# Performance work log

Measured on AMD Instinct MI355X. Metric: run time of the kernel, lower is better.

Reference implementation:

```python
import jax, jax.numpy as jnp
import numpy as np

N = 50000; E = 800000; H = 4; C = 64; FEAT = 128; EDIM = 16; G = 256
NEG_SLOPE = 0.2; BN_EPS = 1e-5


def _gat_layer(x, src, dst, W, a_src, a_dst, bias, gamma, beta, alpha_edge=None):
    # GATConv (concat=True, PyG math), then BatchNorm1d (batch stats) + ReLU.
    h = (x @ W).reshape(N, H, C)                       # [N,H,C]
    alpha = (h * a_src).sum(-1)[src] + (h * a_dst).sum(-1)[dst]   # [Etot,H]
    if alpha_edge is not None:
        alpha = alpha + alpha_edge
    alpha = jax.nn.leaky_relu(alpha, NEG_SLOPE)
    amax = jax.ops.segment_max(alpha, dst, num_segments=N)        # edge softmax over dst
    ea = jnp.exp(alpha - amax[dst])
    denom = jax.ops.segment_sum(ea, dst, num_segments=N)
    coef = ea / (denom[dst] + 1e-16)
    out = jax.ops.segment_sum(coef[:, :, None] * h[src], dst, num_segments=N)
    out = out.reshape(N, H * C) + bias
    mu = out.mean(0)
    var = out.var(0)
    out = (out - mu) / jnp.sqrt(var + BN_EPS) * gamma + beta
    return jax.nn.relu(out)


def setup_inputs() -> dict:
    key = jax.random.key(0)
    ks = jax.random.split(key, 32)
    s = 0.05
    inp = {
        "x": jax.random.normal(ks[0], (N, FEAT), jnp.float32),
        "edge_index": jax.random.randint(ks[1], (2, E), 0, N),
        "edge_attr": jax.random.normal(ks[2], (E, EDIM), jnp.float32),
        "batch": jnp.sort(jax.random.randint(ks[3], (N,), 0, G)),
    }
    in_dims = [FEAT, H * C, H * C]
    for i in range(3):
        k = 4 + 7 * i
        inp[f"W{i}"] = jax.random.normal(ks[k], (in_dims[i], H * C), jnp.float32) * s
        inp[f"att_src{i}"] = jax.random.normal(ks[k + 1], (H, C), jnp.float32) * s
        inp[f"att_dst{i}"] = jax.random.normal(ks[k + 2], (H, C), jnp.float32) * s
        inp[f"bias{i}"] = jnp.zeros((H * C,), jnp.float32)
        inp[f"gamma{i}"] = jnp.ones((H * C,), jnp.float32)
        inp[f"beta{i}"] = jnp.zeros((H * C,), jnp.float32)
    inp["We0"] = jax.random.normal(ks[28], (EDIM, H * C), jnp.float32) * s
    inp["att_e0"] = jax.random.normal(ks[29], (H, C), jnp.float32) * s
    return inp


def reference(x, edge_index, edge_attr, batch,
              W0, att_src0, att_dst0, bias0, gamma0, beta0,
              W1, att_src1, att_dst1, bias1, gamma1, beta1,
              W2, att_src2, att_dst2, bias2, gamma2, beta2,
              We0, att_e0):
    # PyG GATConv adds self-loops; edge_attr for self-loops filled with mean.
    loops = jnp.arange(N)
    src = jnp.concatenate([edge_index[0], loops])
    dst = jnp.concatenate([edge_index[1], loops])
    ea_sl = jnp.concatenate([edge_attr, jnp.broadcast_to(edge_attr.mean(0), (N, EDIM))], 0)
    e = (ea_sl @ We0).reshape(E + N, H, C)
    alpha_e = (e * att_e0).sum(-1)                     # [Etot,H]
    x = _gat_layer(x, src, dst, W0, att_src0, att_dst0, bias0, gamma0, beta0, alpha_e)
    x = _gat_layer(x, src, dst, W1, att_src1, att_dst1, bias1, gamma1, beta1)
    x = _gat_layer(x, src, dst, W2, att_src2, att_dst2, bias2, gamma2, beta2)
    # global_mean_pool
    counts = jax.ops.segment_sum(jnp.ones((N,), x.dtype), batch, num_segments=G)
    sums = jax.ops.segment_sum(x, batch, num_segments=G)
    return sums / jnp.clip(counts, 1.0)[:, None]
```

## Files before the change

kernel.cpp:

```cpp
#include <hip/hip_runtime.h>
#include <math.h>

#define NN 50000
#define NE 800000
#define ET 850000
#define HCC 256
#define GG 256
#define CAP 64
#define NB 16

constexpr size_t NHC    = (size_t)NN * HCC;
constexpr size_t O_H    = 0;
constexpr size_t O_AGG  = O_H + NHC / 2;
constexpr size_t O_REC  = O_AGG + NHC / 2;
constexpr size_t O_BT0  = O_REC + (size_t)NN * CAP * 4;
constexpr size_t O_BT1  = O_BT0 + 16384;
constexpr size_t O_BT2  = O_BT1 + 32768;
constexpr size_t O_AS   = O_BT2 + 32768;
constexpr size_t O_AD   = O_AS + (size_t)NN * 4;
constexpr size_t O_M    = O_AD + (size_t)NN * 4;
constexpr size_t O_ZERO = O_M + 64;
constexpr size_t O_DEG  = O_ZERO;
constexpr size_t O_SLS  = O_DEG + NN;
constexpr size_t O_PART = O_SLS + 4;
constexpr size_t O_END  = O_PART + 3 * NB * 512;

typedef __attribute__((ext_vector_type(8))) short bf16x8;
typedef __attribute__((ext_vector_type(4))) float f32x4;

__device__ inline unsigned short f2bf(float f) {
    unsigned int u = __float_as_uint(f);
    unsigned int r = (u + 0x7fffu + ((u >> 16) & 1u)) >> 16;
    return (unsigned short)r;
}
__device__ inline float b2f(unsigned short u) {
    return __uint_as_float(((unsigned int)u) << 16);
}
__device__ inline float bflo(unsigned int u) { return __uint_as_float(u << 16); }
__device__ inline float bfhi(unsigned int u) { return __uint_as_float(u & 0xffff0000u); }

__global__ void prep_kernel(const float* __restrict__ W0, const float* __restrict__ W1,
                            const float* __restrict__ W2,
                            const float* __restrict__ We0, const float* __restrict__ att_e0,
                            unsigned short* __restrict__ Bt0,
                            unsigned short* __restrict__ Bt1,
                            unsigned short* __restrict__ Bt2,
                            float* __restrict__ M) {
    int b = blockIdx.x;
    if (b == 640) {
        int t = threadIdx.x;
        if (t < 64) {
            int k = t >> 2, hh = t & 3;
            float s = 0.f;
            for (int c = 0; c < 64; ++c)
                s += We0[k * 256 + hh * 64 + c] * att_e0[hh * 64 + c];
            M[k * 4 + hh] = s;
        }
        return;
    }
    const float* W; unsigned short* Bt; int K, base;
    if (b < 128)      { W = W0; Bt = Bt0; K = 128; base = 0; }
    else if (b < 384) { W = W1; Bt = Bt1; K = 256; base = 128; }
    else              { W = W2; Bt = Bt2; K = 256; base = 384; }
    int idx = (b - base) * 256 + threadIdx.x;
    int n = idx & 255, k = idx >> 8;
    Bt[(size_t)n * K + k] = f2bf(W[(size_t)k * 256 + n]);
}

__global__ void csr_kernel(const int* __restrict__ srcA, const int* __restrict__ dstA,
                           const float* __restrict__ ea, const float* __restrict__ M,
                           int* __restrict__ deg, uint4* __restrict__ rec,
                           float* __restrict__ slsum) {
    int t0 = blockIdx.x * 1024 + threadIdx.x;
    float a0 = 0.f, a1 = 0.f, a2 = 0.f, a3 = 0.f;
    #pragma unroll
    for (int q = 0; q < 4; ++q) {
        int e = t0 + q * 256;
        if (e < ET) {
            bool real = (e < NE);
            int d = real ? dstA[e] : (e - NE);
            int s = real ? srcA[e] : (e - NE);
            int p = atomicAdd(&deg[d], 1);
            if (p > CAP - 1) p = CAP - 1;
            int slot = d * CAP + p;
            uint4 r;
            r.z = (unsigned)s;
            if (real) {
                r.w = 0u;
                const float4* pp = (const float4*)(ea + (size_t)e * 16);
                float4 va = pp[0], vb = pp[1], vc = pp[2], vd = pp[3];
                float v[16] = {va.x, va.y, va.z, va.w, vb.x, vb.y, vb.z, vb.w,
                               vc.x, vc.y, vc.z, vc.w, vd.x, vd.y, vd.z, vd.w};
                float o0 = 0.f, o1 = 0.f, o2 = 0.f, o3 = 0.f;
                #pragma unroll
                for (int k = 0; k < 16; ++k) {
                    float4 m4 = *(const float4*)(M + k * 4);
                    o0 = fmaf(v[k], m4.x, o0);
                    o1 = fmaf(v[k], m4.y, o1);
                    o2 = fmaf(v[k], m4.z, o2);
                    o3 = fmaf(v[k], m4.w, o3);
                }
                r.x = ((unsigned)f2bf(o1) << 16) | (unsigned)f2bf(o0);
                r.y = ((unsigned)f2bf(o3) << 16) | (unsigned)f2bf(o2);
                a0 += o0; a1 += o1; a2 += o2; a3 += o3;
            } else {
                r.x = 0u; r.y = 0u; r.w = 1u;
            }
            rec[slot] = r;
        }
    }
    #pragma unroll
    for (int off = 32; off; off >>= 1) {
        a0 += __shfl_xor(a0, off);
        a1 += __shfl_xor(a1, off);
        a2 += __shfl_xor(a2, off);
        a3 += __shfl_xor(a3, off);
    }
    __shared__ float part[4][4];
    int wave = threadIdx.x >> 6, lane = threadIdx.x & 63;
    if (lane == 0) {
        part[wave][0] = a0; part[wave][1] = a1;
        part[wave][2] = a2; part[wave][3] = a3;
    }
    __syncthreads();
    if (threadIdx.x < 4)
        atomicAdd(&slsum[threadIdx.x],
                  part[0][threadIdx.x] + part[1][threadIdx.x] +
                  part[2][threadIdx.x] + part[3][threadIdx.x]);
}

template <int K, bool NORM>
__global__ __launch_bounds__(256) void gemm_fused(const float* __restrict__ Af,
                                                  const unsigned short* __restrict__ Ab,
                                                  const unsigned short* __restrict__ Bt,
                                                  const float* __restrict__ part,
                                                  const float* __restrict__ gamma,
                                                  const float* __restrict__ beta,
                                                  const float* __restrict__ att_src,
                                                  const float* __restrict__ att_dst,
                                                  unsigned short* __restrict__ Hout,
                                                  float* __restrict__ asA,
                                                  float* __restrict__ adA, int M) {
    __shared__ unsigned short As[64][40];
    __shared__ unsigned short Bs[256][40];
    __shared__ float kvs[256], cvs[256];
    int tid = threadIdx.x;
    int wave = tid >> 6, lane = tid & 63;
    int quad = lane >> 4, l16 = lane & 15;
    int row0 = blockIdx.x * 64;
    f32x4 acc[4][4] = {};

    if (NORM) {
        int ch = tid;
        float s = 0.f, s2 = 0.f;
        #pragma unroll
        for (int b = 0; b < NB; ++b) {
            s  += part[b * 512 + ch];
            s2 += part[b * 512 + 256 + ch];
        }
        const float invN = 1.0f / (float)NN;
        float mr = s * invN;
        float var = s2 * invN - mr * mr;
        float k = gamma[ch] * rsqrtf(var + 1e-5f);
        kvs[ch] = k;
        cvs[ch] = beta[ch] - mr * k;
        __syncthreads();
    }

    for (int k0 = 0; k0 < K; k0 += 32) {
        {
            int row = tid >> 2, seg = tid & 3;
            ushort4 o0 = make_ushort4(0, 0, 0, 0), o1 = o0;
            if (row0 + row < M) {
                float u[8];
                if (NORM) {
                    uint4 raw = *(const uint4*)(Ab + (size_t)(row0 + row) * K + k0 + seg * 8);
                    u[0] = bflo(raw.x); u[1] = bfhi(raw.x);
                    u[2] = bflo(raw.y); u[3] = bfhi(raw.y);
                    u[4] = bflo(raw.z); u[5] = bfhi(raw.z);
                    u[6] = bflo(raw.w); u[7] = bfhi(raw.w);
                    int cb = k0 + seg * 8;
                    #pragma unroll
                    for (int q = 0; q < 8; ++q)
                        u[q] = fmaxf(fmaf(u[q], kvs[cb + q], cvs[cb + q]), 0.f);
                } else {
                    const float* ap = Af + (size_t)(row0 + row) * K + k0 + seg * 8;
                    float4 f1 = *(const float4*)ap;
                    float4 f2 = *(const float4*)(ap + 4);
                    u[0] = f1.x; u[1] = f1.y; u[2] = f1.z; u[3] = f1.w;
                    u[4] = f2.x; u[5] = f2.y; u[6] = f2.z; u[7] = f2.w;
                }
                o0 = make_ushort4(f2bf(u[0]), f2bf(u[1]), f2bf(u[2]), f2bf(u[3]));
                o1 = make_ushort4(f2bf(u[4]), f2bf(u[5]), f2bf(u[6]), f2bf(u[7]));
            }
            *(ushort4*)&As[row][seg * 8] = o0;
            *(ushort4*)&As[row][seg * 8 + 4] = o1;
        }
        {
            const uint4* src = (const uint4*)(Bt + (size_t)tid * K + k0);
            uint4 b0 = src[0], b1 = src[1], b2 = src[2], b3 = src[3];
            uint4* dst = (uint4*)&Bs[tid][0];
            dst[0] = b0; dst[1] = b1; dst[2] = b2; dst[3] = b3;
        }
        __syncthreads();
        bf16x8 a_frag[4], b_frag[4];
        #pragma unroll
        for (int mi = 0; mi < 4; ++mi)
            a_frag[mi] = *(const bf16x8*)&As[mi * 16 + l16][quad * 8];
        #pragma unroll
        for (int ni = 0; ni < 4; ++ni)
            b_frag[ni] = *(const bf16x8*)&Bs[wave * 64 + ni * 16 + l16][quad * 8];
        #pragma unroll
        for (int mi = 0; mi < 4; ++mi)
            #pragma unroll
            for (int ni = 0; ni < 4; ++ni)
                acc[mi][ni] = __builtin_amdgcn_mfma_f32_16x16x32_bf16(
                    a_frag[mi], b_frag[ni], acc[mi][ni], 0, 0, 0);
        __syncthreads();
    }

    #pragma unroll
    for (int mi = 0; mi < 4; ++mi) {
        #pragma unroll
        for (int reg = 0; reg < 4; ++reg) {
            int r = row0 + mi * 16 + quad * 4 + reg;
            if (r < M) {
                #pragma unroll
                for (int ni = 0; ni < 4; ++ni) {
                    int c = wave * 64 + ni * 16 + l16;
                    Hout[(size_t)r * HCC + c] = f2bf(acc[mi][ni][reg]);
                }
            }
        }
    }
    float asc[4], adc_[4];
    #pragma unroll
    for (int ni = 0; ni < 4; ++ni) {
        asc[ni] = att_src[wave * 64 + ni * 16 + l16];
        adc_[ni] = att_dst[wave * 64 + ni * 16 + l16];
    }
    #pragma unroll
    for (int mi = 0; mi < 4; ++mi) {
        #pragma unroll
        for (int reg = 0; reg < 4; ++reg) {
            float s1 = acc[mi][0][reg] * asc[0] + acc[mi][1][reg] * asc[1] +
                       acc[mi][2][reg] * asc[2] + acc[mi][3][reg] * asc[3];
            float d1 = acc[mi][0][reg] * adc_[0] + acc[mi][1][reg] * adc_[1] +
                       acc[mi][2][reg] * adc_[2] + acc[mi][3][reg] * adc_[3];
            #pragma unroll
            for (int off = 1; off < 16; off <<= 1) {
                s1 += __shfl_xor(s1, off);
                d1 += __shfl_xor(d1, off);
            }
            int r = row0 + mi * 16 + quad * 4 + reg;
            if (l16 == 0 && r < M) {
                asA[(size_t)r * 4 + wave] = s1;
                adA[(size_t)r * 4 + wave] = d1;
            }
        }
    }
}

template <bool HAS_AE>
__global__ __launch_bounds__(256) void agg_kernel(const unsigned short* __restrict__ Hm,
                                                  const float* __restrict__ asA,
                                                  const float* __restrict__ adA,
                                                  const uint4* __restrict__ rec,
                                                  const int* __restrict__ degA,
                                                  const float* __restrict__ slsum,
                                                  unsigned short* __restrict__ outA,
                                                  float* __restrict__ part) {
    __shared__ float wlds[4][260];
    __shared__ float slds[2][4][256];
    int wave = threadIdx.x >> 6, lane = threadIdx.x & 63;
    int n = blockIdx.x * 4 + wave;
    int head = lane >> 4;
    int st = n * CAP;
    int d = degA[n];
    if (d > CAP) d = CAP;
    float4 ad4 = *(const float4*)(adA + (size_t)n * 4);

    float4 w4 = make_float4(0.f, 0.f, 0.f, 0.f);
    int ms = 0;
    if (lane < d) {
        uint4 r = rec[st + lane];
        ms = (int)r.z;
        float4 av = *(const float4*)(asA + (size_t)ms * 4);
        float4 t = make_float4(av.x + ad4.x, av.y + ad4.y, av.z + ad4.z, av.w + ad4.w);
        if (HAS_AE) {
            if (r.w) {
                const float inv = 1.0f / (float)NE;
                t.x += slsum[0] * inv; t.y += slsum[1] * inv;
                t.z += slsum[2] * inv; t.w += slsum[3] * inv;
            } else {
                t.x += bflo(r.x); t.y += bfhi(r.x);
                t.z += bflo(r.y); t.w += bfhi(r.y);
            }
        }
        t.x = (t.x > 0.f) ? t.x : 0.2f * t.x;
        t.y = (t.y > 0.f) ? t.y : 0.2f * t.y;
        t.z = (t.z > 0.f) ? t.z : 0.2f * t.z;
        t.w = (t.w > 0.f) ? t.w : 0.2f * t.w;
        w4.x = __expf(t.x);
        w4.y = __expf(t.y);
        w4.z = __expf(t.z);
        w4.w = __expf(t.w);
    }
    float4 Dv = w4;
    wlds[wave][0 * 65 + lane] = w4.x;
    wlds[wave][1 * 65 + lane] = w4.y;
    wlds[wave][2 * 65 + lane] = w4.z;
    wlds[wave][3 * 65 + lane] = w4.w;

    float4 acc = make_float4(0.f, 0.f, 0.f, 0.f);
    const unsigned short* hb = Hm + lane * 4;
    int cnt8 = (d + 7) & ~7;
    const float* wrow = &wlds[wave][head * 65];
    for (int jj = 0; jj < cnt8; jj += 8) {
        int sj[8];
        #pragma unroll
        for (int q = 0; q < 8; ++q)
            sj[q] = __builtin_amdgcn_readlane(ms, jj + q);
        ushort4 hv[8];
        #pragma unroll
        for (int q = 0; q < 8; ++q)
            hv[q] = *(const ushort4*)(hb + (size_t)sj[q] * HCC);
        float wq[8];
        #pragma unroll
        for (int q = 0; q < 8; ++q)
            wq[q] = wrow[jj + q];
        #pragma unroll
        for (int q = 0; q < 8; ++q) {
            acc.x = fmaf(wq[q], b2f(hv[q].x), acc.x);
            acc.y = fmaf(wq[q], b2f(hv[q].y), acc.y);
            acc.z = fmaf(wq[q], b2f(hv[q].z), acc.z);
            acc.w = fmaf(wq[q], b2f(hv[q].w), acc.w);
        }
    }
    #pragma unroll
    for (int off = 32; off; off >>= 1) {
        Dv.x += __shfl_xor(Dv.x, off);
        Dv.y += __shfl_xor(Dv.y, off);
        Dv.z += __shfl_xor(Dv.z, off);
        Dv.w += __shfl_xor(Dv.w, off);
    }
    float D = (head & 2) ? ((head & 1) ? Dv.w : Dv.z) : ((head & 1) ? Dv.y : Dv.x);
    float inv = 1.0f / (D + 1e-16f);
    float4 o = make_float4(acc.x * inv, acc.y * inv, acc.z * inv, acc.w * inv);
    ushort4 ob = make_ushort4(f2bf(o.x), f2bf(o.y), f2bf(o.z), f2bf(o.w));
    *(ushort4*)(outA + (size_t)n * HCC + lane * 4) = ob;

    *(float4*)&slds[0][wave][lane * 4] = o;
    *(float4*)&slds[1][wave][lane * 4] =
        make_float4(o.x * o.x, o.y * o.y, o.z * o.z, o.w * o.w);
    __syncthreads();
    int t = threadIdx.x;
    float s  = slds[0][0][t] + slds[0][1][t] + slds[0][2][t] + slds[0][3][t];
    float s2 = slds[1][0][t] + slds[1][1][t] + slds[1][2][t] + slds[1][3][t];
    int bucket = blockIdx.x & (NB - 1);
    atomicAdd(&part[bucket * 512 + t], s);
    atomicAdd(&part[bucket * 512 + 256 + t], s2);
}

__global__ void pool_kernel(const unsigned short* __restrict__ aggb,
                            const float* __restrict__ part,
                            const float* __restrict__ gamma, const float* __restrict__ beta,
                            const int* __restrict__ batch,
                            float* __restrict__ out) {
    int ch = threadIdx.x;
    int g = blockIdx.x;
    float s = 0.f, s2 = 0.f;
    #pragma unroll
    for (int b = 0; b < NB; ++b) {
        s  += part[b * 512 + ch];
        s2 += part[b * 512 + 256 + ch];
    }
    const float invN = 1.0f / (float)NN;
    float mr = s * invN;
    float var = s2 * invN - mr * mr;
    float k = gamma[ch] * rsqrtf(var + 1e-5f);
    float c = beta[ch] - mr * k;

    int lo = 0, hi = NN;
    while (lo < hi) { int mid = (lo + hi) >> 1; if (batch[mid] < g) lo = mid + 1; else hi = mid; }
    int start = lo;
    lo = start; hi = NN;
    while (lo < hi) { int mid = (lo + hi) >> 1; if (batch[mid] < g + 1) lo = mid + 1; else hi = mid; }
    int end = lo;

    float a0 = 0.f, a1 = 0.f, a2 = 0.f, a3 = 0.f;
    int n = start;
    for (; n + 3 < end; n += 4) {
        a0 += fmaxf(fmaf(b2f(aggb[(size_t)n * HCC + ch]), k, c), 0.f);
        a1 += fmaxf(fmaf(b2f(aggb[(size_t)(n + 1) * HCC + ch]), k, c), 0.f);
        a2 += fmaxf(fmaf(b2f(aggb[(size_t)(n + 2) * HCC + ch]), k, c), 0.f);
        a3 += fmaxf(fmaf(b2f(aggb[(size_t)(n + 3) * HCC + ch]), k, c), 0.f);
    }
    for (; n < end; ++n)
        a0 += fmaxf(fmaf(b2f(aggb[(size_t)n * HCC + ch]), k, c), 0.f);
    float tot = (a0 + a1) + (a2 + a3);
    out[(size_t)g * HCC + ch] = tot / fmaxf((float)(end - start), 1.0f);
}

extern "C" void kernel_launch(void* const* d_in, const int* in_sizes, int n_in,
                              void* d_out, int out_size, void* d_ws, size_t ws_size,
                              hipStream_t stream) {
    const float* x = (const float*)d_in[0];
    const int* edge_index = (const int*)d_in[1];
    const int* srcA = edge_index;
    const int* dstA = edge_index + NE;
    const float* edge_attr = (const float*)d_in[2];
    const int* batch = (const int*)d_in[3];
    const float* W[3]   = {(const float*)d_in[4],  (const float*)d_in[10], (const float*)d_in[16]};
    const float* asc[3] = {(const float*)d_in[5],  (const float*)d_in[11], (const float*)d_in[17]};
    const float* adc[3] = {(const float*)d_in[6],  (const float*)d_in[12], (const float*)d_in[18]};
    const float* gam[3] = {(const float*)d_in[8],  (const float*)d_in[14], (const float*)d_in[20]};
    const float* bet[3] = {(const float*)d_in[9],  (const float*)d_in[15], (const float*)d_in[21]};
    const float* We0 = (const float*)d_in[22];
    const float* att_e0 = (const float*)d_in[23];

    float* wsf = (float*)d_ws;
    unsigned short* hbuf = (unsigned short*)(wsf + O_H);
    unsigned short* aggb = (unsigned short*)(wsf + O_AGG);
    uint4* rec   = (uint4*)(wsf + O_REC);
    unsigned short* Bt0  = (unsigned short*)(wsf + O_BT0);
    unsigned short* Bt1  = (unsigned short*)(wsf + O_BT1);
    unsigned short* Bt2  = (unsigned short*)(wsf + O_BT2);
    float* asA   = wsf + O_AS;
    float* adA   = wsf + O_AD;
    float* Mb    = wsf + O_M;
    int*   deg   = (int*)(wsf + O_DEG);
    float* slsum = wsf + O_SLS;
    float* part  = wsf + O_PART;

    hipMemsetAsync((void*)(wsf + O_ZERO), 0, (O_END - O_ZERO) * sizeof(float), stream);

    prep_kernel<<<641, 256, 0, stream>>>(W[0], W[1], W[2], We0, att_e0, Bt0, Bt1, Bt2, Mb);
    csr_kernel<<<(ET + 1023) / 1024, 256, 0, stream>>>(srcA, dstA, edge_attr, Mb,
                                                       deg, rec, slsum);

    unsigned short* Bts[3] = {Bt0, Bt1, Bt2};
    for (int L = 0; L < 3; ++L) {
        if (L == 0)
            gemm_fused<128, false><<<782, 256, 0, stream>>>(x, (const unsigned short*)0,
                Bts[0], (const float*)0, gam[0], bet[0], asc[0], adc[0], hbuf, asA, adA, NN);
        else
            gemm_fused<256, true><<<782, 256, 0, stream>>>((const float*)0, aggb,
                Bts[L], part + (size_t)(L - 1) * NB * 512, gam[L - 1], bet[L - 1],
                asc[L], adc[L], hbuf, asA, adA, NN);
        if (L == 0)
            agg_kernel<true><<<12500, 256, 0, stream>>>(hbuf, asA, adA, rec, deg, slsum,
                aggb, part + (size_t)L * NB * 512);
        else
            agg_kernel<false><<<12500, 256, 0, stream>>>(hbuf, asA, adA, rec, deg, slsum,
                aggb, part + (size_t)L * NB * 512);
    }

    pool_kernel<<<GG, 256, 0, stream>>>(aggb, part + (size_t)2 * NB * 512,
                                        gam[2], bet[2], batch, (float*)d_out);
}
```

Measured before the change: 544.2 us.

## Fold zeroing into prep, widen agg blocks, prefetch neighbor rows, double csr work

The workspace memset is replaced by extra blocks in prep_kernel that zero the region with float4 stores, saving a separate launch. csr_kernel now handles 8 edges per thread instead of 4. agg_kernel grows to 512 threads covering 8 nodes per block, which halves the BN-partial atomics per node. Its neighbor loop now loads the next batch of 8 bf16 rows before accumulating the current one. The prefetch raises register pressure and larger blocks may hurt occupancy scheduling.

```diff
diff --git a/kernel.cpp b/kernel.cpp
--- a/kernel.cpp
+++ b/kernel.cpp
@@ -24,6 +24,8 @@
 constexpr size_t O_SLS  = O_DEG + NN;
 constexpr size_t O_PART = O_SLS + 4;
 constexpr size_t O_END  = O_PART + 3 * NB * 512;
+constexpr size_t ZWORDS = O_END - O_ZERO;
+constexpr int    ZBLK   = (int)((ZWORDS / 4 + 255) / 256);
 
 typedef __attribute__((ext_vector_type(8))) short bf16x8;
 typedef __attribute__((ext_vector_type(4))) float f32x4;
@@ -45,8 +47,14 @@
                             unsigned short* __restrict__ Bt0,
                             unsigned short* __restrict__ Bt1,
                             unsigned short* __restrict__ Bt2,
-                            float* __restrict__ M) {
+                            float* __restrict__ M, float* __restrict__ zbase) {
     int b = blockIdx.x;
+    if (b >= 641) {
+        size_t idx = ((size_t)(b - 641) * 256 + threadIdx.x) * 4;
+        if (idx < ZWORDS)
+            *(float4*)(zbase + idx) = make_float4(0.f, 0.f, 0.f, 0.f);
+        return;
+    }
     if (b == 640) {
         int t = threadIdx.x;
         if (t < 64) {
@@ -71,10 +79,10 @@
                            const float* __restrict__ ea, const float* __restrict__ M,
                            int* __restrict__ deg, uint4* __restrict__ rec,
                            float* __restrict__ slsum) {
-    int t0 = blockIdx.x * 1024 + threadIdx.x;
+    int t0 = blockIdx.x * 2048 + threadIdx.x;
     float a0 = 0.f, a1 = 0.f, a2 = 0.f, a3 = 0.f;
     #pragma unroll
-    for (int q = 0; q < 4; ++q) {
+    for (int q = 0; q < 8; ++q) {
         int e = t0 + q * 256;
         if (e < ET) {
             bool real = (e < NE);
@@ -262,7 +270,7 @@
 }
 
 template <bool HAS_AE>
-__global__ __launch_bounds__(256) void agg_kernel(const unsigned short* __restrict__ Hm,
+__global__ __launch_bounds__(512) void agg_kernel(const unsigned short* __restrict__ Hm,
                                                   const float* __restrict__ asA,
                                                   const float* __restrict__ adA,
                                                   const uint4* __restrict__ rec,
@@ -270,10 +278,10 @@
                                                   const float* __restrict__ slsum,
                                                   unsigned short* __restrict__ outA,
                                                   float* __restrict__ part) {
-    __shared__ float wlds[4][260];
-    __shared__ float slds[2][4][256];
+    __shared__ float wlds[8][260];
+    __shared__ float slds[2][8][256];
     int wave = threadIdx.x >> 6, lane = threadIdx.x & 63;
-    int n = blockIdx.x * 4 + wave;
+    int n = blockIdx.x * 8 + wave;
     int head = lane >> 4;
     int st = n * CAP;
     int d = degA[n];
@@ -316,25 +324,42 @@
     const unsigned short* hb = Hm + lane * 4;
     int cnt8 = (d + 7) & ~7;
     const float* wrow = &wlds[wave][head * 65];
+
+    int sjA[8]; ushort4 hvA[8];
+    #pragma unroll
+    for (int q = 0; q < 8; ++q)
+        sjA[q] = __builtin_amdgcn_readlane(ms, q);
+    #pragma unroll
+    for (int q = 0; q < 8; ++q)
+        hvA[q] = *(const ushort4*)(hb + (size_t)sjA[q] * HCC);
     for (int jj = 0; jj < cnt8; jj += 8) {
-        int sj[8];
-        #pragma unroll
-        for (int q = 0; q < 8; ++q)
-            sj[q] = __builtin_amdgcn_readlane(ms, jj + q);
-        ushort4 hv[8];
-        #pragma unroll
-        for (int q = 0; q < 8; ++q)
-            hv[q] = *(const ushort4*)(hb + (size_t)sj[q] * HCC);
+        int nj = jj + 8;
+        bool more = (nj < cnt8);
+        ushort4 hvB[8];
+        if (more) {
+            int sjB[8];
+            #pragma unroll
+            for (int q = 0; q < 8; ++q)
+                sjB[q] = __builtin_amdgcn_readlane(ms, nj + q);
+            #pragma unroll
+            for (int q = 0; q < 8; ++q)
+                hvB[q] = *(const ushort4*)(hb + (size_t)sjB[q] * HCC);
+        }
         float wq[8];
         #pragma unroll
         for (int q = 0; q < 8; ++q)
             wq[q] = wrow[jj + q];
         #pragma unroll
         for (int q = 0; q < 8; ++q) {
-            acc.x = fmaf(wq[q], b2f(hv[q].x), acc.x);
-            acc.y = fmaf(wq[q], b2f(hv[q].y), acc.y);
-            acc.z = fmaf(wq[q], b2f(hv[q].z), acc.z);
-            acc.w = fmaf(wq[q], b2f(hv[q].w), acc.w);
+            acc.x = fmaf(wq[q], b2f(hvA[q].x), acc.x);
+            acc.y = fmaf(wq[q], b2f(hvA[q].y), acc.y);
+            acc.z = fmaf(wq[q], b2f(hvA[q].z), acc.z);
+            acc.w = fmaf(wq[q], b2f(hvA[q].w), acc.w);
+        }
+        if (more) {
+            #pragma unroll
+            for (int q = 0; q < 8; ++q)
+                hvA[q] = hvB[q];
         }
     }
     #pragma unroll
@@ -355,11 +380,15 @@
         make_float4(o.x * o.x, o.y * o.y, o.z * o.z, o.w * o.w);
     __syncthreads();
     int t = threadIdx.x;
-    float s  = slds[0][0][t] + slds[0][1][t] + slds[0][2][t] + slds[0][3][t];
-    float s2 = slds[1][0][t] + slds[1][1][t] + slds[1][2][t] + slds[1][3][t];
-    int bucket = blockIdx.x & (NB - 1);
-    atomicAdd(&part[bucket * 512 + t], s);
-    atomicAdd(&part[bucket * 512 + 256 + t], s2);
+    if (t < 512) {
+        int ch = t & 255, which = t >> 8;
+        float s = 0.f;
+        #pragma unroll
+        for (int w = 0; w < 8; ++w)
+            s += slds[which][w][ch];
+        int bucket = blockIdx.x & (NB - 1);
+        atomicAdd(&part[bucket * 512 + which * 256 + ch], s);
+    }
 }
 
 __global__ void pool_kernel(const unsigned short* __restrict__ aggb,
@@ -433,10 +462,9 @@
     float* slsum = wsf + O_SLS;
     float* part  = wsf + O_PART;
 
-    hipMemsetAsync((void*)(wsf + O_ZERO), 0, (O_END - O_ZERO) * sizeof(float), stream);
-
-    prep_kernel<<<641, 256, 0, stream>>>(W[0], W[1], W[2], We0, att_e0, Bt0, Bt1, Bt2, Mb);
-    csr_kernel<<<(ET + 1023) / 1024, 256, 0, stream>>>(srcA, dstA, edge_attr, Mb,
+    prep_kernel<<<641 + ZBLK, 256, 0, stream>>>(W[0], W[1], W[2], We0, att_e0,
+                                                Bt0, Bt1, Bt2, Mb, wsf + O_ZERO);
+    csr_kernel<<<(ET + 2047) / 2048, 256, 0, stream>>>(srcA, dstA, edge_attr, Mb,
                                                        deg, rec, slsum);
 
     unsigned short* Bts[3] = {Bt0, Bt1, Bt2};
@@ -449,10 +477,10 @@
                 Bts[L], part + (size_t)(L - 1) * NB * 512, gam[L - 1], bet[L - 1],
                 asc[L], adc[L], hbuf, asA, adA, NN);
         if (L == 0)
-            agg_kernel<true><<<12500, 256, 0, stream>>>(hbuf, asA, adA, rec, deg, slsum,
+            agg_kernel<true><<<6250, 512, 0, stream>>>(hbuf, asA, adA, rec, deg, slsum,
                 aggb, part + (size_t)L * NB * 512);
         else
-            agg_kernel<false><<<12500, 256, 0, stream>>>(hbuf, asA, adA, rec, deg, slsum,
+            agg_kernel<false><<<6250, 512, 0, stream>>>(hbuf, asA, adA, rec, deg, slsum,
                 aggb, part + (size_t)L * NB * 512);
     }
 
```

Result: faster. 529.7 us (-2.7%).
